# Kernel optimization log

Measured on AMD Instinct MI355X. Metric: run time of the kernel, lower is better.

## Reference

```python
import jax, jax.numpy as jnp
import numpy as np

B, N, K = 16, 1024, 20
BOX = 10.0
IN_DIM = 78
HID = 128


def setup_inputs() -> dict:
    key = jax.random.key(0)
    k1, k2, k3, k4, k5 = jax.random.split(key, 5)
    position = jax.random.uniform(k1, (B, N, 3), dtype=jnp.float32) * BOX
    # random proper orthonormal orientation matrices via QR
    R_raw = jax.random.normal(k2, (B, N, 3, 3), dtype=jnp.float32)
    orientation_R, _ = jnp.linalg.qr(R_raw)
    w1 = jax.random.normal(k3, (IN_DIM, HID), jnp.float32) * (1.0 / np.sqrt(IN_DIM))
    b1 = jnp.zeros((HID,), jnp.float32)
    w2 = jax.random.normal(k4, (HID, HID), jnp.float32) * (1.0 / np.sqrt(HID))
    b2 = jnp.zeros((HID,), jnp.float32)
    w3 = jax.random.normal(k5, (HID, 1), jnp.float32) * (1.0 / np.sqrt(HID))
    b3 = jnp.zeros((1,), jnp.float32)
    return dict(position=position, orientation_R=orientation_R,
                w1=w1, b1=b1, w2=w2, b2=b2, w3=w3, b3=b3)


def _features(position, orientation_R):
    # all-pairs displacement with minimum-image periodic boundary
    dr = position[:, :, None, :] - position[:, None, :, :]        # (B,N,N,3)
    dr = dr - BOX * jnp.round(dr / BOX)
    r2 = jnp.sum(dr * dr, axis=-1)                                # (B,N,N)
    r2 = r2 + jnp.eye(N, dtype=r2.dtype) * 1e9                    # exclude self
    neg_r2, idx = jax.lax.top_k(-r2, K)                           # (B,N,K)
    NN_R = jnp.sqrt(-neg_r2)[..., None]                           # (B,N,K,1)
    NN_dr = jnp.take_along_axis(dr, idx[..., None], axis=2)       # (B,N,K,3)
    u = NN_dr / NN_R                                              # unit separation
    inv_r = 1.0 / NN_R
    bidx = jnp.arange(B)[:, None, None]
    Rn = orientation_R[bidx, idx]                                 # (B,N,K,3,3) neighbor frames
    Rp = orientation_R                                            # (B,N,3,3) particle frame
    # pairwise dot products of principal axes: (B,N,K,3,3)
    dot = jnp.einsum('bnij,bnklj->bnkil', Rp, Rn)
    # elementwise products of every axis pair: (B,N,K,3,3,3)
    elem = Rp[:, :, None, :, None, :] * Rn[:, :, :, None, :, :]
    elem_norm = jnp.linalg.norm(elem, axis=-1)                    # (B,N,K,3,3)
    # cross products of corresponding principal axes: (B,N,K,3,3)
    cross = jnp.cross(Rp[:, :, None, :, :], Rn)
    cross_norm = jnp.linalg.norm(cross, axis=-1)                  # (B,N,K,3)
    # relative orientation R_i^T R_j: (B,N,K,3,3)
    rel = jnp.einsum('bnji,bnkjl->bnkil', Rp, Rn)
    # RBF of dr projected on principal axes
    rbf_p = jnp.exp(-jnp.einsum('bnkd,bnid->bnki', u, Rp) ** 2)   # (B,N,K,3)
    rbf_n = jnp.exp(-jnp.einsum('bnkd,bnkid->bnki', u, Rn) ** 2)  # (B,N,K,3)
    tr = rel[..., 0, 0] + rel[..., 1, 1] + rel[..., 2, 2]
    angle = jnp.arccos(jnp.clip((tr - 1.0) * 0.5, -1.0 + 1e-6, 1.0 - 1e-6))[..., None]
    feats = jnp.concatenate([
        NN_R, inv_r, u,
        dot.reshape(B, N, K, 9),
        elem.reshape(B, N, K, 27),
        elem_norm.reshape(B, N, K, 9),
        cross.reshape(B, N, K, 9),
        cross_norm,
        rel.reshape(B, N, K, 9),
        rbf_p, rbf_n, angle,
    ], axis=-1)                                                   # (B,N,K,78)
    return feats


def reference(position, orientation_R, w1, b1, w2, b2, w3, b3):
    f = _features(position, orientation_R)                        # (B,N,K,78)
    h = jnp.tanh(f @ w1 + b1)
    h = jnp.tanh(h @ w2 + b2)
    pooled = jnp.max(h, axis=2)                                   # max-pool over neighbors
    energy = pooled @ w3 + b3                                     # (B,N,1)
    return energy
```

## Files before the change

### kernel.cpp

```cpp
#include <hip/hip_runtime.h>
#include <hip/hip_bf16.h>

namespace {

constexpr int B = 16;
constexpr int N = 1024;
constexpr int K = 20;
constexpr int HID = 128;
constexpr float BOX = 10.0f;

constexpr int PPB = 4;
constexpr int MROWS = PPB * K;
constexpr int MT = 5;
constexpr int KP1 = 96;
constexpr int FP = 104;
constexpr int H1P = 136;
constexpr int SURVCAP = 128;
constexpr int NTHR = 8;

constexpr float THRC[NTHR] = {1.5625f, 3.0625f, 5.0625f, 7.5625f,
                              10.5625f, 14.0625f, 18.0625f, 76.0f};

constexpr int GRID_SEL  = B * N / PPB;
constexpr int CONV_ELEMS = 128 * KP1 + 128 * 128;
constexpr int GRID_CONV = (CONV_ELEMS + 255) / 256;

typedef __attribute__((ext_vector_type(8))) short short8;
typedef __attribute__((ext_vector_type(4))) float f32x4;

__device__ __forceinline__ float tanh_f(float x) {
    float e = __expf(2.0f * x);
    return 1.0f - 2.0f / (e + 1.0f);
}

__device__ __forceinline__ ushort bfb(float x) {
    __hip_bfloat16 h = __float2bfloat16(x);
    return __builtin_bit_cast(ushort, h);
}

__device__ __forceinline__ float pbc(float d) {
    const float hi = __fsub_rn(d, BOX);
    const float lo = __fadd_rn(d, BOX);
    return d > 5.0f ? hi : (d < -5.0f ? lo : d);
}

__global__ __launch_bounds__(256, 8) void select_kernel(
    const float* __restrict__ pos,
    const float* __restrict__ w1, const float* __restrict__ w2,
    ushort* __restrict__ w1Th, ushort* __restrict__ w1Tl,
    ushort* __restrict__ w2Th, ushort* __restrict__ w2Tl,
    ushort* __restrict__ nbr)
{
    const int t = threadIdx.x;

    if (blockIdx.x >= GRID_SEL) {
        const int idx = (blockIdx.x - GRID_SEL) * 256 + t;
        if (idx < 128 * KP1) {
            const int n = idx / KP1, k = idx - n * KP1;
            const float v = (k < 78) ? w1[k * HID + n] : 0.0f;
            const __hip_bfloat16 h = __float2bfloat16(v);
            w1Th[idx] = __builtin_bit_cast(ushort, h);
            w1Tl[idx] = bfb(v - __bfloat162float(h));
        } else if (idx < CONV_ELEMS) {
            const int i = idx - 128 * KP1;
            const int n = i >> 7, k = i & 127;
            const float v = w2[k * HID + n];
            const __hip_bfloat16 h = __float2bfloat16(v);
            w2Th[i] = __builtin_bit_cast(ushort, h);
            w2Tl[i] = bfb(v - __bfloat162float(h));
        }
        return;
    }

    __shared__ ushort cntS[4][PPB][NTHR];
    __shared__ unsigned long long survS[PPB][SURVCAP];
    __shared__ float thrS[PPB];
    __shared__ uint  scntS[PPB];

    const int pid0 = blockIdx.x * PPB;
    const int b  = pid0 >> 10;
    const int nb = pid0 & (N - 1);
    const float* posb = pos + (size_t)b * N * 3;

    if (t < PPB) scntS[t] = 0;

    float cx[PPB], cy[PPB], cz[PPB];
#pragma unroll
    for (int p = 0; p < PPB; ++p) {
        cx[p] = posb[(nb + p) * 3 + 0];
        cy[p] = posb[(nb + p) * 3 + 1];
        cz[p] = posb[(nb + p) * 3 + 2];
    }

    float r2v[PPB][4];
#pragma unroll
    for (int q = 0; q < 4; ++q) {
        const int j = t + q * 256;
        const float px = posb[j * 3 + 0];
        const float py = posb[j * 3 + 1];
        const float pz = posb[j * 3 + 2];
#pragma unroll
        for (int p = 0; p < PPB; ++p) {
            const float dx = pbc(__fsub_rn(cx[p], px));
            const float dy = pbc(__fsub_rn(cy[p], py));
            const float dz = pbc(__fsub_rn(cz[p], pz));
            float r2 = __fadd_rn(__fadd_rn(__fmul_rn(dx, dx), __fmul_rn(dy, dy)),
                                 __fmul_rn(dz, dz));
            if (j == nb + p) r2 = 1e9f;
            r2v[p][q] = r2;
        }
    }

    {
        const int wv = t >> 6, lane = t & 63;
#pragma unroll
        for (int p = 0; p < PPB; ++p) {
#pragma unroll
            for (int i = 0; i < NTHR; ++i) {
                uint c = 0;
#pragma unroll
                for (int q = 0; q < 4; ++q)
                    c += (uint)__popcll(__ballot(r2v[p][q] < THRC[i]));
                if (lane == 0) cntS[wv][p][i] = (ushort)c;
            }
        }
    }
    __syncthreads();

    {
        const int p = t >> 6, lane = t & 63;
        uint tot = 0;
        float thrv = 0.0f;
        if (lane < NTHR) {
            tot = (uint)cntS[0][p][lane] + cntS[1][p][lane]
                + (uint)cntS[2][p][lane] + cntS[3][p][lane];
#pragma unroll
            for (int i = 0; i < NTHR; ++i) if (lane == i) thrv = THRC[i];
        }
        const unsigned long long m = __ballot(lane < NTHR && tot >= (uint)K);
        const int sel = __ffsll((long long)m) - 1;
        if (lane == sel) thrS[p] = thrv;
    }
    __syncthreads();

#pragma unroll
    for (int p = 0; p < PPB; ++p) {
        const float thr = thrS[p];
#pragma unroll
        for (int q = 0; q < 4; ++q) {
            if (r2v[p][q] < thr) {
                const uint pp = atomicAdd(&scntS[p], 1u);
                if (pp < (uint)SURVCAP)
                    survS[p][pp] = ((unsigned long long)__float_as_uint(r2v[p][q]) << 32)
                                   | (uint)(t + q * 256);
            }
        }
    }
    __syncthreads();

    {
        const int p = t >> 6;
        const int S = min((int)scntS[p], SURVCAP);
#pragma unroll
        for (int half = 0; half < 2; ++half) {
            const int s = (t & 63) + half * 64;
            if (s < S) {
                const unsigned long long me = survS[p][s];
                int rank = 0;
                for (int jj = 0; jj < S; ++jj) rank += (survS[p][jj] < me) ? 1 : 0;
                if (rank < K)
                    nbr[(size_t)(pid0 + p) * K + rank] = (ushort)(me & 0xffffULL);
            }
        }
    }
}

__global__ __launch_bounds__(256, 7) void mlp_kernel(
    const float* __restrict__ pos, const float* __restrict__ ori,
    const float* __restrict__ b1, const float* __restrict__ b2,
    const float* __restrict__ w3, const float* __restrict__ b3,
    const ushort* __restrict__ w1Th, const ushort* __restrict__ w1Tl,
    const ushort* __restrict__ w2Th, const ushort* __restrict__ w2Tl,
    const ushort* __restrict__ nbr, float* __restrict__ out)
{
    __shared__ __align__(16) char uS[MROWS * H1P * 2];
    __hip_bfloat16 (*const fS)[FP] = (__hip_bfloat16 (*)[FP])uS;
    ushort (*const h1S)[H1P] = (ushort (*)[H1P])uS;
    __shared__ float RpS[PPB][9];
    __shared__ float red[4][PPB];

    const int pid0 = blockIdx.x * PPB;
    const int b  = pid0 >> 10;
    const int nb = pid0 & (N - 1);
    const int t  = threadIdx.x;
    const float* posb = pos + (size_t)b * N * 3;
    const float* orib = ori + (size_t)b * N * 9;

    if (t < PPB * 9) RpS[t / 9][t % 9] = orib[(size_t)(nb + t / 9) * 9 + (t % 9)];
    __syncthreads();

    if (t < PPB * K) {
        const int p = t / K, k = t - p * K;
        const int j = (int)nbr[(size_t)(pid0 + p) * K + k];
        float Rp[9], Rn[9];
#pragma unroll
        for (int q = 0; q < 9; ++q) Rp[q] = RpS[p][q];
#pragma unroll
        for (int q = 0; q < 9; ++q) Rn[q] = orib[(size_t)j * 9 + q];

        const float cxp = posb[(nb + p) * 3 + 0];
        const float cyp = posb[(nb + p) * 3 + 1];
        const float czp = posb[(nb + p) * 3 + 2];
        const float dx = pbc(__fsub_rn(cxp, posb[j * 3 + 0]));
        const float dy = pbc(__fsub_rn(cyp, posb[j * 3 + 1]));
        const float dz = pbc(__fsub_rn(czp, posb[j * 3 + 2]));
        const float r2 = __fadd_rn(__fadd_rn(__fmul_rn(dx, dx), __fmul_rn(dy, dy)),
                                   __fmul_rn(dz, dz));
        const float r = sqrtf(r2);
        const float invr = 1.0f / r;
        const float ux = dx * invr, uy = dy * invr, uz = dz * invr;

        __hip_bfloat16* f = fS[p * K + k];
        f[0] = __float2bfloat16(r);
        f[1] = __float2bfloat16(invr);
        f[2] = __float2bfloat16(ux);
        f[3] = __float2bfloat16(uy);
        f[4] = __float2bfloat16(uz);

        float diag[3];
#pragma unroll
        for (int i = 0; i < 3; ++i) {
#pragma unroll
            for (int l = 0; l < 3; ++l) {
                float s = 0.0f, en2 = 0.0f;
#pragma unroll
                for (int m = 0; m < 3; ++m) {
                    const float e = Rp[i * 3 + m] * Rn[l * 3 + m];
                    f[14 + i * 9 + l * 3 + m] = __float2bfloat16(e);
                    en2 += e * e;
                    s += e;
                }
                f[5 + i * 3 + l] = __float2bfloat16(s);
                f[41 + i * 3 + l] = __float2bfloat16(sqrtf(en2));
                float rr = 0.0f;
#pragma unroll
                for (int m = 0; m < 3; ++m) rr += Rp[m * 3 + i] * Rn[m * 3 + l];
                f[62 + i * 3 + l] = __float2bfloat16(rr);
                if (i == l) diag[i] = rr;
            }
        }
#pragma unroll
        for (int i = 0; i < 3; ++i) {
            const float ax = Rp[i * 3 + 0], ay = Rp[i * 3 + 1], az = Rp[i * 3 + 2];
            const float bx = Rn[i * 3 + 0], by = Rn[i * 3 + 1], bz = Rn[i * 3 + 2];
            const float ccx = ay * bz - az * by;
            const float ccy = az * bx - ax * bz;
            const float ccz = ax * by - ay * bx;
            f[50 + i * 3 + 0] = __float2bfloat16(ccx);
            f[50 + i * 3 + 1] = __float2bfloat16(ccy);
            f[50 + i * 3 + 2] = __float2bfloat16(ccz);
            f[59 + i] = __float2bfloat16(sqrtf(ccx * ccx + ccy * ccy + ccz * ccz));
            const float dp = ux * ax + uy * ay + uz * az;
            f[71 + i] = __float2bfloat16(__expf(-dp * dp));
            const float dn = ux * bx + uy * by + uz * bz;
            f[74 + i] = __float2bfloat16(__expf(-dn * dn));
        }
        const float tr = diag[0] + diag[1] + diag[2];
        float ca = (tr - 1.0f) * 0.5f;
        ca = fminf(fmaxf(ca, -1.0f + 1e-6f), 1.0f - 1e-6f);
        f[77] = __float2bfloat16(acosf(ca));
#pragma unroll
        for (int i = 78; i < KP1; ++i) f[i] = __float2bfloat16(0.0f);
    }
    __syncthreads();

    const int wv = t >> 6, ln = t & 63;
    const int lr = ln & 15, lg = ln >> 4;
    const int n0 = wv * 32 + lr, n1 = n0 + 16;

    f32x4 acc[MT][2];
    {
        const float bb0 = b1[n0], bb1 = b1[n1];
#pragma unroll
        for (int mt = 0; mt < MT; ++mt) {
            acc[mt][0] = f32x4{bb0, bb0, bb0, bb0};
            acc[mt][1] = f32x4{bb1, bb1, bb1, bb1};
        }
    }
    {
        const ushort* pb0h = w1Th + n0 * KP1 + lg * 8;
        const ushort* pb0l = w1Tl + n0 * KP1 + lg * 8;
        const ushort* pb1h = w1Th + n1 * KP1 + lg * 8;
        const ushort* pb1l = w1Tl + n1 * KP1 + lg * 8;
#pragma unroll
        for (int ks = 0; ks < 3; ++ks) {
            const short8 b0h = *reinterpret_cast<const short8*>(pb0h + ks * 32);
            const short8 b0l = *reinterpret_cast<const short8*>(pb0l + ks * 32);
            const short8 b1h = *reinterpret_cast<const short8*>(pb1h + ks * 32);
            const short8 b1l = *reinterpret_cast<const short8*>(pb1l + ks * 32);
#pragma unroll
            for (int mt = 0; mt < MT; ++mt) {
                const short8 a = *reinterpret_cast<const short8*>(
                    &fS[16 * mt + lr][ks * 32 + lg * 8]);
                acc[mt][0] = __builtin_amdgcn_mfma_f32_16x16x32_bf16(a, b0h, acc[mt][0], 0, 0, 0);
                acc[mt][0] = __builtin_amdgcn_mfma_f32_16x16x32_bf16(a, b0l, acc[mt][0], 0, 0, 0);
                acc[mt][1] = __builtin_amdgcn_mfma_f32_16x16x32_bf16(a, b1h, acc[mt][1], 0, 0, 0);
                acc[mt][1] = __builtin_amdgcn_mfma_f32_16x16x32_bf16(a, b1l, acc[mt][1], 0, 0, 0);
            }
        }
    }
    __syncthreads();
#pragma unroll
    for (int mt = 0; mt < MT; ++mt)
#pragma unroll
        for (int r = 0; r < 4; ++r) {
            h1S[16 * mt + 4 * lg + r][n0] = bfb(tanh_f(acc[mt][0][r]));
            h1S[16 * mt + 4 * lg + r][n1] = bfb(tanh_f(acc[mt][1][r]));
        }
    __syncthreads();

    {
        const float bb0 = b2[n0], bb1 = b2[n1];
#pragma unroll
        for (int mt = 0; mt < MT; ++mt) {
            acc[mt][0] = f32x4{bb0, bb0, bb0, bb0};
            acc[mt][1] = f32x4{bb1, bb1, bb1, bb1};
        }
    }
    {
        const ushort* pb0h = w2Th + n0 * HID + lg * 8;
        const ushort* pb0l = w2Tl + n0 * HID + lg * 8;
        const ushort* pb1h = w2Th + n1 * HID + lg * 8;
        const ushort* pb1l = w2Tl + n1 * HID + lg * 8;
#pragma unroll
        for (int ks = 0; ks < 4; ++ks) {
            const short8 b0h = *reinterpret_cast<const short8*>(pb0h + ks * 32);
            const short8 b0l = *reinterpret_cast<const short8*>(pb0l + ks * 32);
            const short8 b1h = *reinterpret_cast<const short8*>(pb1h + ks * 32);
            const short8 b1l = *reinterpret_cast<const short8*>(pb1l + ks * 32);
#pragma unroll
            for (int mt = 0; mt < MT; ++mt) {
                const short8 a = *reinterpret_cast<const short8*>(
                    &h1S[16 * mt + lr][ks * 32 + lg * 8]);
                acc[mt][0] = __builtin_amdgcn_mfma_f32_16x16x32_bf16(a, b0h, acc[mt][0], 0, 0, 0);
                acc[mt][0] = __builtin_amdgcn_mfma_f32_16x16x32_bf16(a, b0l, acc[mt][0], 0, 0, 0);
                acc[mt][1] = __builtin_amdgcn_mfma_f32_16x16x32_bf16(a, b1h, acc[mt][1], 0, 0, 0);
                acc[mt][1] = __builtin_amdgcn_mfma_f32_16x16x32_bf16(a, b1l, acc[mt][1], 0, 0, 0);
            }
        }
    }

#pragma unroll
    for (int mt = 0; mt < MT; ++mt)
#pragma unroll
        for (int nt = 0; nt < 2; ++nt)
#pragma unroll
            for (int r = 0; r < 4; ++r) acc[mt][nt][r] = tanh_f(acc[mt][nt][r]);

    const float w3n0 = w3[n0], w3n1 = w3[n1];
#pragma unroll
    for (int p = 0; p < PPB; ++p) {
        float m0 = -3.0e38f, m1 = -3.0e38f;
#pragma unroll
        for (int mt = 0; mt < MT; ++mt) {
            const bool in = (uint)(4 * mt + lg - 5 * p) < 5u;
#pragma unroll
            for (int r = 0; r < 4; ++r) {
                m0 = fmaxf(m0, in ? acc[mt][0][r] : -3.0e38f);
                m1 = fmaxf(m1, in ? acc[mt][1][r] : -3.0e38f);
            }
        }
        m0 = fmaxf(m0, __shfl_xor(m0, 16, 64));
        m0 = fmaxf(m0, __shfl_xor(m0, 32, 64));
        m1 = fmaxf(m1, __shfl_xor(m1, 16, 64));
        m1 = fmaxf(m1, __shfl_xor(m1, 32, 64));
        float v = m0 * w3n0 + m1 * w3n1;
#pragma unroll
        for (int off = 1; off < 16; off <<= 1) v += __shfl_xor(v, off, 64);
        if (ln == 0) red[wv][p] = v;
    }
    __syncthreads();
    if (t < PPB) out[pid0 + t] = red[0][t] + red[1][t] + red[2][t] + red[3][t] + b3[0];
}

}

extern "C" void kernel_launch(void* const* d_in, const int* in_sizes, int n_in,
                              void* d_out, int out_size, void* d_ws, size_t ws_size,
                              hipStream_t stream) {
    const float* pos = (const float*)d_in[0];
    const float* ori = (const float*)d_in[1];
    const float* w1  = (const float*)d_in[2];
    const float* b1  = (const float*)d_in[3];
    const float* w2  = (const float*)d_in[4];
    const float* b2  = (const float*)d_in[5];
    const float* w3  = (const float*)d_in[6];
    const float* b3  = (const float*)d_in[7];
    float* out = (float*)d_out;

    ushort* w1Th = (ushort*)d_ws;
    ushort* w1Tl = w1Th + 128 * KP1;
    ushort* w2Th = w1Tl + 128 * KP1;
    ushort* w2Tl = w2Th + 128 * 128;
    ushort* nbr  = w2Tl + 128 * 128;

    select_kernel<<<dim3(GRID_SEL + GRID_CONV), dim3(256), 0, stream>>>(
        pos, w1, w2, w1Th, w1Tl, w2Th, w2Tl, nbr);
    mlp_kernel<<<dim3(GRID_SEL), dim3(256), 0, stream>>>(
        pos, ori, b1, b2, w3, b3, w1Th, w1Tl, w2Th, w2Tl, nbr, out);
}
```

Before: 165.8 us.

## Fuse neighbor selection into MLP kernel and split weight conversion into its own kernel

Neighbor selection and the feature/MLP stage now run in one kernel per block of 4 particles, and the neighbor list is kept in shared memory instead of a global round trip. The survivor buffer aliases the feature/hidden shared buffer, and particle positions held in registers are reused. Weight conversion becomes a separate small kernel. The MFMA loops are restructured to process one output tile at a time, which may reduce register pressure. Occupancy bounds drop to 5 blocks per SM, so the longer kernel may hide latency less well.

```diff
diff --git a/kernel.cpp b/kernel.cpp
--- a/kernel.cpp
+++ b/kernel.cpp
@@ -44,45 +44,57 @@
     return d > 5.0f ? hi : (d < -5.0f ? lo : d);
 }
 
-__global__ __launch_bounds__(256, 8) void select_kernel(
-    const float* __restrict__ pos,
+__global__ __launch_bounds__(256) void conv_w_kernel(
     const float* __restrict__ w1, const float* __restrict__ w2,
     ushort* __restrict__ w1Th, ushort* __restrict__ w1Tl,
-    ushort* __restrict__ w2Th, ushort* __restrict__ w2Tl,
-    ushort* __restrict__ nbr)
+    ushort* __restrict__ w2Th, ushort* __restrict__ w2Tl)
 {
-    const int t = threadIdx.x;
-
-    if (blockIdx.x >= GRID_SEL) {
-        const int idx = (blockIdx.x - GRID_SEL) * 256 + t;
-        if (idx < 128 * KP1) {
-            const int n = idx / KP1, k = idx - n * KP1;
-            const float v = (k < 78) ? w1[k * HID + n] : 0.0f;
-            const __hip_bfloat16 h = __float2bfloat16(v);
-            w1Th[idx] = __builtin_bit_cast(ushort, h);
-            w1Tl[idx] = bfb(v - __bfloat162float(h));
-        } else if (idx < CONV_ELEMS) {
-            const int i = idx - 128 * KP1;
-            const int n = i >> 7, k = i & 127;
-            const float v = w2[k * HID + n];
-            const __hip_bfloat16 h = __float2bfloat16(v);
-            w2Th[i] = __builtin_bit_cast(ushort, h);
-            w2Tl[i] = bfb(v - __bfloat162float(h));
-        }
-        return;
-    }
+    const int idx = blockIdx.x * 256 + threadIdx.x;
+    if (idx < 128 * KP1) {
+        const int n = idx / KP1, k = idx - n * KP1;
+        const float v = (k < 78) ? w1[k * HID + n] : 0.0f;
+        const __hip_bfloat16 h = __float2bfloat16(v);
+        w1Th[idx] = __builtin_bit_cast(ushort, h);
+        w1Tl[idx] = bfb(v - __bfloat162float(h));
+    } else if (idx < CONV_ELEMS) {
+        const int i = idx - 128 * KP1;
+        const int n = i >> 7, k = i & 127;
+        const float v = w2[k * HID + n];
+        const __hip_bfloat16 h = __float2bfloat16(v);
+        w2Th[i] = __builtin_bit_cast(ushort, h);
+        w2Tl[i] = bfb(v - __bfloat162float(h));
+    }
+}
+
+__global__ __launch_bounds__(256, 5) void fused_kernel(
+    const float* __restrict__ pos, const float* __restrict__ ori,
+    const float* __restrict__ b1, const float* __restrict__ b2,
+    const float* __restrict__ w3, const float* __restrict__ b3,
+    const ushort* __restrict__ w1Th, const ushort* __restrict__ w1Tl,
+    const ushort* __restrict__ w2Th, const ushort* __restrict__ w2Tl,
+    float* __restrict__ out)
+{
+    __shared__ __align__(16) char uS[MROWS * H1P * 2];
+    __hip_bfloat16 (*const fS)[FP] = (__hip_bfloat16 (*)[FP])uS;
+    ushort (*const h1S)[H1P] = (ushort (*)[H1P])uS;
+    unsigned long long* const survS = (unsigned long long*)uS;
 
     __shared__ ushort cntS[4][PPB][NTHR];
-    __shared__ unsigned long long survS[PPB][SURVCAP];
-    __shared__ float thrS[PPB];
-    __shared__ uint  scntS[PPB];
+    __shared__ ushort nbrS[PPB][K];
+    __shared__ float  RpS[PPB][9];
+    __shared__ float  red[4][PPB];
+    __shared__ float  thrS[PPB];
+    __shared__ uint   scntS[PPB];
 
     const int pid0 = blockIdx.x * PPB;
     const int b  = pid0 >> 10;
     const int nb = pid0 & (N - 1);
+    const int t  = threadIdx.x;
     const float* posb = pos + (size_t)b * N * 3;
+    const float* orib = ori + (size_t)b * N * 9;
 
     if (t < PPB) scntS[t] = 0;
+    if (t < PPB * 9) RpS[t / 9][t % 9] = orib[(size_t)(nb + t / 9) * 9 + (t % 9)];
 
     float cx[PPB], cy[PPB], cz[PPB];
 #pragma unroll
@@ -151,8 +163,9 @@
             if (r2v[p][q] < thr) {
                 const uint pp = atomicAdd(&scntS[p], 1u);
                 if (pp < (uint)SURVCAP)
-                    survS[p][pp] = ((unsigned long long)__float_as_uint(r2v[p][q]) << 32)
-                                   | (uint)(t + q * 256);
+                    survS[p * SURVCAP + pp] =
+                        ((unsigned long long)__float_as_uint(r2v[p][q]) << 32)
+                        | (uint)(t + q * 256);
             }
         }
     }
@@ -161,59 +174,32 @@
     {
         const int p = t >> 6;
         const int S = min((int)scntS[p], SURVCAP);
+        const unsigned long long* sp = survS + p * SURVCAP;
 #pragma unroll
         for (int half = 0; half < 2; ++half) {
             const int s = (t & 63) + half * 64;
             if (s < S) {
-                const unsigned long long me = survS[p][s];
+                const unsigned long long me = sp[s];
                 int rank = 0;
-                for (int jj = 0; jj < S; ++jj) rank += (survS[p][jj] < me) ? 1 : 0;
-                if (rank < K)
-                    nbr[(size_t)(pid0 + p) * K + rank] = (ushort)(me & 0xffffULL);
-            }
-        }
-    }
-}
-
-__global__ __launch_bounds__(256, 7) void mlp_kernel(
-    const float* __restrict__ pos, const float* __restrict__ ori,
-    const float* __restrict__ b1, const float* __restrict__ b2,
-    const float* __restrict__ w3, const float* __restrict__ b3,
-    const ushort* __restrict__ w1Th, const ushort* __restrict__ w1Tl,
-    const ushort* __restrict__ w2Th, const ushort* __restrict__ w2Tl,
-    const ushort* __restrict__ nbr, float* __restrict__ out)
-{
-    __shared__ __align__(16) char uS[MROWS * H1P * 2];
-    __hip_bfloat16 (*const fS)[FP] = (__hip_bfloat16 (*)[FP])uS;
-    ushort (*const h1S)[H1P] = (ushort (*)[H1P])uS;
-    __shared__ float RpS[PPB][9];
-    __shared__ float red[4][PPB];
-
-    const int pid0 = blockIdx.x * PPB;
-    const int b  = pid0 >> 10;
-    const int nb = pid0 & (N - 1);
-    const int t  = threadIdx.x;
-    const float* posb = pos + (size_t)b * N * 3;
-    const float* orib = ori + (size_t)b * N * 9;
-
-    if (t < PPB * 9) RpS[t / 9][t % 9] = orib[(size_t)(nb + t / 9) * 9 + (t % 9)];
+                for (int jj = 0; jj < S; ++jj) rank += (sp[jj] < me) ? 1 : 0;
+                if (rank < K) nbrS[p][rank] = (ushort)(me & 0xffffULL);
+            }
+        }
+    }
     __syncthreads();
 
     if (t < PPB * K) {
         const int p = t / K, k = t - p * K;
-        const int j = (int)nbr[(size_t)(pid0 + p) * K + k];
+        const int j = (int)nbrS[p][k];
         float Rp[9], Rn[9];
 #pragma unroll
         for (int q = 0; q < 9; ++q) Rp[q] = RpS[p][q];
 #pragma unroll
         for (int q = 0; q < 9; ++q) Rn[q] = orib[(size_t)j * 9 + q];
 
-        const float cxp = posb[(nb + p) * 3 + 0];
-        const float cyp = posb[(nb + p) * 3 + 1];
-        const float czp = posb[(nb + p) * 3 + 2];
-        const float dx = pbc(__fsub_rn(cxp, posb[j * 3 + 0]));
-        const float dy = pbc(__fsub_rn(cyp, posb[j * 3 + 1]));
-        const float dz = pbc(__fsub_rn(czp, posb[j * 3 + 2]));
+        const float dx = pbc(__fsub_rn(cx[p], posb[j * 3 + 0]));
+        const float dy = pbc(__fsub_rn(cy[p], posb[j * 3 + 1]));
+        const float dz = pbc(__fsub_rn(cz[p], posb[j * 3 + 2]));
         const float r2 = __fadd_rn(__fadd_rn(__fmul_rn(dx, dx), __fmul_rn(dy, dy)),
                                    __fmul_rn(dz, dz));
         const float r = sqrtf(r2);
@@ -279,33 +265,24 @@
     const int n0 = wv * 32 + lr, n1 = n0 + 16;
 
     f32x4 acc[MT][2];
-    {
-        const float bb0 = b1[n0], bb1 = b1[n1];
-#pragma unroll
-        for (int mt = 0; mt < MT; ++mt) {
-            acc[mt][0] = f32x4{bb0, bb0, bb0, bb0};
-            acc[mt][1] = f32x4{bb1, bb1, bb1, bb1};
-        }
-    }
-    {
-        const ushort* pb0h = w1Th + n0 * KP1 + lg * 8;
-        const ushort* pb0l = w1Tl + n0 * KP1 + lg * 8;
-        const ushort* pb1h = w1Th + n1 * KP1 + lg * 8;
-        const ushort* pb1l = w1Tl + n1 * KP1 + lg * 8;
+#pragma unroll
+    for (int nt = 0; nt < 2; ++nt) {
+        const int nn = (nt == 0) ? n0 : n1;
+        const float bb = b1[nn];
+#pragma unroll
+        for (int mt = 0; mt < MT; ++mt) acc[mt][nt] = f32x4{bb, bb, bb, bb};
+        const ushort* pbh = w1Th + nn * KP1 + lg * 8;
+        const ushort* pbl = w1Tl + nn * KP1 + lg * 8;
 #pragma unroll
         for (int ks = 0; ks < 3; ++ks) {
-            const short8 b0h = *reinterpret_cast<const short8*>(pb0h + ks * 32);
-            const short8 b0l = *reinterpret_cast<const short8*>(pb0l + ks * 32);
-            const short8 b1h = *reinterpret_cast<const short8*>(pb1h + ks * 32);
-            const short8 b1l = *reinterpret_cast<const short8*>(pb1l + ks * 32);
+            const short8 bh = *reinterpret_cast<const short8*>(pbh + ks * 32);
+            const short8 bl = *reinterpret_cast<const short8*>(pbl + ks * 32);
 #pragma unroll
             for (int mt = 0; mt < MT; ++mt) {
                 const short8 a = *reinterpret_cast<const short8*>(
                     &fS[16 * mt + lr][ks * 32 + lg * 8]);
-                acc[mt][0] = __builtin_amdgcn_mfma_f32_16x16x32_bf16(a, b0h, acc[mt][0], 0, 0, 0);
-                acc[mt][0] = __builtin_amdgcn_mfma_f32_16x16x32_bf16(a, b0l, acc[mt][0], 0, 0, 0);
-                acc[mt][1] = __builtin_amdgcn_mfma_f32_16x16x32_bf16(a, b1h, acc[mt][1], 0, 0, 0);
-                acc[mt][1] = __builtin_amdgcn_mfma_f32_16x16x32_bf16(a, b1l, acc[mt][1], 0, 0, 0);
+                acc[mt][nt] = __builtin_amdgcn_mfma_f32_16x16x32_bf16(a, bh, acc[mt][nt], 0, 0, 0);
+                acc[mt][nt] = __builtin_amdgcn_mfma_f32_16x16x32_bf16(a, bl, acc[mt][nt], 0, 0, 0);
             }
         }
     }
@@ -319,33 +296,24 @@
         }
     __syncthreads();
 
-    {
-        const float bb0 = b2[n0], bb1 = b2[n1];
-#pragma unroll
-        for (int mt = 0; mt < MT; ++mt) {
-            acc[mt][0] = f32x4{bb0, bb0, bb0, bb0};
-            acc[mt][1] = f32x4{bb1, bb1, bb1, bb1};
-        }
-    }
-    {
-        const ushort* pb0h = w2Th + n0 * HID + lg * 8;
-        const ushort* pb0l = w2Tl + n0 * HID + lg * 8;
-        const ushort* pb1h = w2Th + n1 * HID + lg * 8;
-        const ushort* pb1l = w2Tl + n1 * HID + lg * 8;
+#pragma unroll
+    for (int nt = 0; nt < 2; ++nt) {
+        const int nn = (nt == 0) ? n0 : n1;
+        const float bb = b2[nn];
+#pragma unroll
+        for (int mt = 0; mt < MT; ++mt) acc[mt][nt] = f32x4{bb, bb, bb, bb};
+        const ushort* pbh = w2Th + nn * HID + lg * 8;
+        const ushort* pbl = w2Tl + nn * HID + lg * 8;
 #pragma unroll
         for (int ks = 0; ks < 4; ++ks) {
-            const short8 b0h = *reinterpret_cast<const short8*>(pb0h + ks * 32);
-            const short8 b0l = *reinterpret_cast<const short8*>(pb0l + ks * 32);
-            const short8 b1h = *reinterpret_cast<const short8*>(pb1h + ks * 32);
-            const short8 b1l = *reinterpret_cast<const short8*>(pb1l + ks * 32);
+            const short8 bh = *reinterpret_cast<const short8*>(pbh + ks * 32);
+            const short8 bl = *reinterpret_cast<const short8*>(pbl + ks * 32);
 #pragma unroll
             for (int mt = 0; mt < MT; ++mt) {
                 const short8 a = *reinterpret_cast<const short8*>(
                     &h1S[16 * mt + lr][ks * 32 + lg * 8]);
-                acc[mt][0] = __builtin_amdgcn_mfma_f32_16x16x32_bf16(a, b0h, acc[mt][0], 0, 0, 0);
-                acc[mt][0] = __builtin_amdgcn_mfma_f32_16x16x32_bf16(a, b0l, acc[mt][0], 0, 0, 0);
-                acc[mt][1] = __builtin_amdgcn_mfma_f32_16x16x32_bf16(a, b1h, acc[mt][1], 0, 0, 0);
-                acc[mt][1] = __builtin_amdgcn_mfma_f32_16x16x32_bf16(a, b1l, acc[mt][1], 0, 0, 0);
+                acc[mt][nt] = __builtin_amdgcn_mfma_f32_16x16x32_bf16(a, bh, acc[mt][nt], 0, 0, 0);
+                acc[mt][nt] = __builtin_amdgcn_mfma_f32_16x16x32_bf16(a, bl, acc[mt][nt], 0, 0, 0);
             }
         }
     }
@@ -402,10 +370,9 @@
     ushort* w1Tl = w1Th + 128 * KP1;
     ushort* w2Th = w1Tl + 128 * KP1;
     ushort* w2Tl = w2Th + 128 * 128;
-    ushort* nbr  = w2Tl + 128 * 128;
-
-    select_kernel<<<dim3(GRID_SEL + GRID_CONV), dim3(256), 0, stream>>>(
-        pos, w1, w2, w1Th, w1Tl, w2Th, w2Tl, nbr);
-    mlp_kernel<<<dim3(GRID_SEL), dim3(256), 0, stream>>>(
-        pos, ori, b1, b2, w3, b3, w1Th, w1Tl, w2Th, w2Tl, nbr, out);
-}
+
+    conv_w_kernel<<<dim3(GRID_CONV), dim3(256), 0, stream>>>(
+        w1, w2, w1Th, w1Tl, w2Th, w2Tl);
+    fused_kernel<<<dim3(GRID_SEL), dim3(256), 0, stream>>>(
+        pos, ori, b1, b2, w3, b3, w1Th, w1Tl, w2Th, w2Tl, out);
+}
```

Result: no change. 166.0 us (+0.1%).
